# Kernel tuning notes

Hardware: AMD Instinct MI355X
Metric: run time of the kernel (lower is better)

## Reference

```python
import jax, jax.numpy as jnp
import numpy as np

N, DEG, D_FEAT, D_OUT = 50000, 32, 128, 256

def setup_inputs() -> dict:
    key = jax.random.key(0)
    k1, k2, k3 = jax.random.split(key, 3)
    features = jax.random.normal(k1, (N, D_FEAT), dtype=jnp.float32)
    edge_look_up = jax.random.randint(k2, (N, DEG), 0, N, dtype=jnp.int64)
    # glorot-uniform kernel, shape (2*D_FEAT, D_OUT)
    limit = np.sqrt(6.0 / (2 * D_FEAT + D_OUT)).astype(np.float32)
    kernel = jax.random.uniform(k3, (2 * D_FEAT, D_OUT), dtype=jnp.float32,
                                minval=-limit, maxval=limit)
    return {"features": features, "edge_look_up": edge_look_up, "kernel": kernel}

def reference(features, edge_look_up, kernel):
    # [1] neighborhood aggregation: gather neighbor features and mean-reduce
    neigh = features[edge_look_up]          # [N, DEG, D_FEAT] (irregular gather)
    agg = jnp.mean(neigh, axis=1)           # [N, D_FEAT]
    # [2] concat self features with aggregated neighbor vectors
    out = jnp.concatenate([features, agg], axis=-1)  # [N, 2*D_FEAT]
    # [4] dense matmul + [5] relu activation
    return jax.nn.relu(out @ kernel)        # [N, D_OUT]
```

## Files before the change

kernel.cpp:

```cpp
#include <hip/hip_runtime.h>

#define NN  50000
#define DEG 32
#define DF  128
#define DO  256
#define FEAT4 (NN * DF / 4)

typedef __bf16 bf16x8 __attribute__((ext_vector_type(8)));
typedef float  f32x4  __attribute__((ext_vector_type(4)));
typedef float  f32x2  __attribute__((ext_vector_type(2)));
typedef unsigned short u16x8 __attribute__((ext_vector_type(8)));

#if defined(__has_builtin)
#if __has_builtin(__builtin_amdgcn_cvt_pk_f32_fp8) && __has_builtin(__builtin_amdgcn_cvt_pk_fp8_f32)
#define HW_FP8 1
#endif
#endif
#ifndef HW_FP8
#define HW_FP8 0
#endif

__device__ __forceinline__ unsigned short f2bf(float f) {
    unsigned u = __float_as_uint(f);
    u += 0x7FFF + ((u >> 16) & 1);
    return (unsigned short)(u >> 16);
}
__device__ __forceinline__ unsigned pkbf(float a, float b) {
    return (unsigned)f2bf(a) | ((unsigned)f2bf(b) << 16);
}

#if !HW_FP8
__device__ __forceinline__ unsigned enc1_fp8(float f) {
    unsigned u = __float_as_uint(f);
    unsigned s = (u >> 31) << 7;
    float a = fabsf(f);
    if (!(a > 0.f)) return s;
    if (a >= 448.f) return s | 0x7E;
    u = __float_as_uint(a);
    int e = (int)((u >> 23) & 255) - 127;
    if (e < -6) {
        unsigned m = (unsigned)(a * 512.f + 0.5f);
        if (m >= 8) return s | 0x08;
        return s | m;
    }
    unsigned mant = (u >> 20) & 7;
    unsigned rnd  = ((u >> 19) & 1) & (((u & 0x7FFFF) != 0) | ((u >> 20) & 1));
    unsigned enc  = ((unsigned)(e + 7) << 3) | mant;
    return s | (enc + rnd);
}
__device__ __forceinline__ float dec1_fp8(unsigned b) {
    unsigned s = (b >> 7) & 1, e = (b >> 3) & 15, m = b & 7;
    float v = (e == 0) ? (float)m * 0.001953125f
                       : __uint_as_float(((e - 7 + 127) << 23) | (m << 20));
    return s ? -v : v;
}
#endif

__device__ __forceinline__ unsigned enc4_fp8(float4 v) {
#if HW_FP8
    int pk = 0;
    pk = __builtin_amdgcn_cvt_pk_fp8_f32(v.x, v.y, pk, false);
    pk = __builtin_amdgcn_cvt_pk_fp8_f32(v.z, v.w, pk, true);
    return (unsigned)pk;
#else
    return enc1_fp8(v.x) | (enc1_fp8(v.y) << 8) | (enc1_fp8(v.z) << 16) | (enc1_fp8(v.w) << 24);
#endif
}

__global__ __launch_bounds__(256) void convert_kernel(
    const float* __restrict__ feat, const float* __restrict__ W,
    unsigned* __restrict__ feat8, unsigned short* __restrict__ Wt)
{
    const int gid = blockIdx.x * 256 + threadIdx.x;
    if (gid < FEAT4) {
        feat8[gid] = enc4_fp8(((const float4*)feat)[gid]);
    } else {
        const int t = gid - FEAT4;
        if (t < DO * DO) {
            const int n = t >> 8, k = t & 255;
            Wt[n * DO + k] = f2bf(W[k * DO + n]);
        }
    }
}

__global__ __launch_bounds__(256) void agg_kernel(
    const unsigned* __restrict__ feat8,
    const int*      __restrict__ edges,
    unsigned short* __restrict__ aggb)
{
    const int node = blockIdx.x * 16 + (threadIdx.x >> 4);
    const int l    = threadIdx.x & 15;
    const int* e   = edges + node * DEG;

    float a[8] = {0.f, 0.f, 0.f, 0.f, 0.f, 0.f, 0.f, 0.f};
    #pragma unroll
    for (int d = 0; d < DEG; ++d) {
        const int idx = e[d];
        const uint2 pk = *(const uint2*)(feat8 + (size_t)idx * (DF / 4) + l * 2);
#if HW_FP8
        const f32x2 v0 = __builtin_amdgcn_cvt_pk_f32_fp8((int)pk.x, false);
        const f32x2 v1 = __builtin_amdgcn_cvt_pk_f32_fp8((int)pk.x, true);
        const f32x2 v2 = __builtin_amdgcn_cvt_pk_f32_fp8((int)pk.y, false);
        const f32x2 v3 = __builtin_amdgcn_cvt_pk_f32_fp8((int)pk.y, true);
        a[0] += v0[0]; a[1] += v0[1]; a[2] += v1[0]; a[3] += v1[1];
        a[4] += v2[0]; a[5] += v2[1]; a[6] += v3[0]; a[7] += v3[1];
#else
        #pragma unroll
        for (int j = 0; j < 4; ++j) a[j]     += dec1_fp8((pk.x >> (8 * j)) & 255);
        #pragma unroll
        for (int j = 0; j < 4; ++j) a[4 + j] += dec1_fp8((pk.y >> (8 * j)) & 255);
#endif
    }

    const float s = 1.0f / (float)DEG;
    u16x8 o;
    #pragma unroll
    for (int j = 0; j < 8; ++j) o[j] = f2bf(a[j] * s);
    *(u16x8*)(aggb + (size_t)node * DF + l * 8) = o;
}

#define BM  64
#define LDA 264

__global__ __launch_bounds__(256) void gemm_kernel(
    const float*          __restrict__ feat,
    const unsigned short* __restrict__ aggb,
    const unsigned short* __restrict__ Wt,
    float*                __restrict__ out)
{
    __shared__ __align__(16) unsigned short Asw[BM * LDA];

    const int tid  = threadIdx.x;
    const int m0   = blockIdx.x * BM;
    const int wave = tid >> 6, lane = tid & 63;
    const int quad = lane >> 4, lr = lane & 15;
    const int wn   = wave * 64;

    {
        const int row = tid >> 2;
        const int cb  = tid & 3;
        int node = m0 + row;
        if (node >= NN) node = NN - 1;
        const float*          fs = feat + (size_t)node * DF;
        const unsigned short* as = aggb + (size_t)node * DF;
        #pragma unroll
        for (int p = 0; p < 4; ++p) {
            const int c8 = (cb + 4 * p) * 8;
            const float4 x = *(const float4*)(fs + c8);
            const float4 y = *(const float4*)(fs + c8 + 4);
            uint4 o;
            o.x = pkbf(x.x, x.y); o.y = pkbf(x.z, x.w);
            o.z = pkbf(y.x, y.y); o.w = pkbf(y.z, y.w);
            *(uint4*)(Asw + row * LDA + c8) = o;
            *(float4*)(Asw + row * LDA + DF + c8) = *(const float4*)(as + c8);
        }
    }
    __syncthreads();

    f32x4 acc[4][4] = {};
    #pragma unroll 2
    for (int kk = 0; kk < 256; kk += 32) {
        bf16x8 af[4], bfr[4];
        #pragma unroll
        for (int i = 0; i < 4; ++i) {
            af[i]  = *(const bf16x8*)(Asw + (i * 16 + lr) * LDA + kk + quad * 8);
            bfr[i] = *(const bf16x8*)(Wt + (size_t)(wn + i * 16 + lr) * DO + kk + quad * 8);
        }
        #pragma unroll
        for (int mi = 0; mi < 4; ++mi)
            #pragma unroll
            for (int ni = 0; ni < 4; ++ni)
                acc[mi][ni] = __builtin_amdgcn_mfma_f32_16x16x32_bf16(
                    af[mi], bfr[ni], acc[mi][ni], 0, 0, 0);
    }

    #pragma unroll
    for (int mi = 0; mi < 4; ++mi) {
        #pragma unroll
        for (int r = 0; r < 4; ++r) {
            const int row = m0 + mi * 16 + quad * 4 + r;
            if (row < NN) {
                #pragma unroll
                for (int ni = 0; ni < 4; ++ni) {
                    out[(size_t)row * DO + wn + ni * 16 + lr] =
                        fmaxf(acc[mi][ni][r], 0.f);
                }
            }
        }
    }
}

extern "C" void kernel_launch(void* const* d_in, const int* in_sizes, int n_in,
                              void* d_out, int out_size, void* d_ws, size_t ws_size,
                              hipStream_t stream)
{
    const float* feat  = (const float*)d_in[0];
    const int*   edges = (const int*)d_in[1];
    const float* W     = (const float*)d_in[2];
    float*       out   = (float*)d_out;

    unsigned short* aggb  = (unsigned short*)d_ws;
    unsigned*       feat8 = (unsigned*)(aggb + (size_t)NN * DF);
    unsigned short* Wt    = (unsigned short*)(feat8 + (size_t)NN * DF / 4);

    convert_kernel<<<(FEAT4 + DO * DO + 255) / 256, 256, 0, stream>>>(feat, W, feat8, Wt);
    agg_kernel<<<NN / 16, 256, 0, stream>>>(feat8, edges, aggb);
    gemm_kernel<<<(NN + BM - 1) / BM, 256, 0, stream>>>(feat, aggb, Wt, out);
}
```

Measured before the change: 132.1 us.

## Precompute bf16 features and load GEMM A operands directly from global memory

The convert kernel now also writes a bf16 copy of the features. The GEMM reads its A fragments straight from global memory (bf16 features for the first half of K, the bf16 aggregate for the second half) instead of staging a converted tile in LDS behind a barrier, and the K loop is fully unrolled. This removes the LDS staging, the in-GEMM conversion and the __syncthreads. In exchange it adds an extra 12.8 MB write plus re-read of featb, and each of the four waves in a block now loads the same A rows from global or cache separately, so redundant global traffic goes up.

```diff
diff --git a/kernel.cpp b/kernel.cpp
--- a/kernel.cpp
+++ b/kernel.cpp
@@ -24,9 +24,6 @@
     unsigned u = __float_as_uint(f);
     u += 0x7FFF + ((u >> 16) & 1);
     return (unsigned short)(u >> 16);
-}
-__device__ __forceinline__ unsigned pkbf(float a, float b) {
-    return (unsigned)f2bf(a) | ((unsigned)f2bf(b) << 16);
 }
 
 #if !HW_FP8
@@ -69,11 +66,16 @@
 
 __global__ __launch_bounds__(256) void convert_kernel(
     const float* __restrict__ feat, const float* __restrict__ W,
-    unsigned* __restrict__ feat8, unsigned short* __restrict__ Wt)
+    unsigned* __restrict__ feat8, unsigned short* __restrict__ featb,
+    unsigned short* __restrict__ Wt)
 {
     const int gid = blockIdx.x * 256 + threadIdx.x;
     if (gid < FEAT4) {
-        feat8[gid] = enc4_fp8(((const float4*)feat)[gid]);
+        const float4 v = ((const float4*)feat)[gid];
+        feat8[gid] = enc4_fp8(v);
+        ushort4 o;
+        o.x = f2bf(v.x); o.y = f2bf(v.y); o.z = f2bf(v.z); o.w = f2bf(v.w);
+        ((ushort4*)featb)[gid] = o;
     } else {
         const int t = gid - FEAT4;
         if (t < DO * DO) {
@@ -119,51 +121,31 @@
     *(u16x8*)(aggb + (size_t)node * DF + l * 8) = o;
 }
 
-#define BM  64
-#define LDA 264
+#define BM 64
 
 __global__ __launch_bounds__(256) void gemm_kernel(
-    const float*          __restrict__ feat,
+    const unsigned short* __restrict__ featb,
     const unsigned short* __restrict__ aggb,
     const unsigned short* __restrict__ Wt,
     float*                __restrict__ out)
 {
-    __shared__ __align__(16) unsigned short Asw[BM * LDA];
-
     const int tid  = threadIdx.x;
     const int m0   = blockIdx.x * BM;
     const int wave = tid >> 6, lane = tid & 63;
     const int quad = lane >> 4, lr = lane & 15;
     const int wn   = wave * 64;
 
-    {
-        const int row = tid >> 2;
-        const int cb  = tid & 3;
-        int node = m0 + row;
-        if (node >= NN) node = NN - 1;
-        const float*          fs = feat + (size_t)node * DF;
-        const unsigned short* as = aggb + (size_t)node * DF;
-        #pragma unroll
-        for (int p = 0; p < 4; ++p) {
-            const int c8 = (cb + 4 * p) * 8;
-            const float4 x = *(const float4*)(fs + c8);
-            const float4 y = *(const float4*)(fs + c8 + 4);
-            uint4 o;
-            o.x = pkbf(x.x, x.y); o.y = pkbf(x.z, x.w);
-            o.z = pkbf(y.x, y.y); o.w = pkbf(y.z, y.w);
-            *(uint4*)(Asw + row * LDA + c8) = o;
-            *(float4*)(Asw + row * LDA + DF + c8) = *(const float4*)(as + c8);
-        }
-    }
-    __syncthreads();
+    f32x4 acc[4][4] = {};
 
-    f32x4 acc[4][4] = {};
-    #pragma unroll 2
+    #pragma unroll
     for (int kk = 0; kk < 256; kk += 32) {
+        const unsigned short* Asrc = (kk < DF) ? (featb + kk) : (aggb + (kk - DF));
         bf16x8 af[4], bfr[4];
         #pragma unroll
         for (int i = 0; i < 4; ++i) {
-            af[i]  = *(const bf16x8*)(Asw + (i * 16 + lr) * LDA + kk + quad * 8);
+            int row = m0 + i * 16 + lr;
+            if (row >= NN) row = NN - 1;
+            af[i]  = *(const bf16x8*)(Asrc + (size_t)row * DF + quad * 8);
             bfr[i] = *(const bf16x8*)(Wt + (size_t)(wn + i * 16 + lr) * DO + kk + quad * 8);
         }
         #pragma unroll
@@ -201,9 +183,11 @@
 
     unsigned short* aggb  = (unsigned short*)d_ws;
     unsigned*       feat8 = (unsigned*)(aggb + (size_t)NN * DF);
-    unsigned short* Wt    = (unsigned short*)(feat8 + (size_t)NN * DF / 4);
+    unsigned short* featb = (unsigned short*)(feat8 + (size_t)NN * DF / 4);
+    unsigned short* Wt    = featb + (size_t)NN * DF;
 
-    convert_kernel<<<(FEAT4 + DO * DO + 255) / 256, 256, 0, stream>>>(feat, W, feat8, Wt);
+    convert_kernel<<<(FEAT4 + DO * DO + 255) / 256, 256, 0, stream>>>(
+        feat, W, feat8, featb, Wt);
     agg_kernel<<<NN / 16, 256, 0, stream>>>(feat8, edges, aggb);
-    gemm_kernel<<<(NN + BM - 1) / BM, 256, 0, stream>>>(feat, aggb, Wt, out);
+    gemm_kernel<<<(NN + BM - 1) / BM, 256, 0, stream>>>(featb, aggb, Wt, out);
 }
```

New measurement: 144.2 us. +9.2%, slower.
